# Performance work log

Measured on AMD Instinct MI355X. Metric: run time of the kernel, lower is better.

The kernel has to match this reference:

```python
import jax, jax.numpy as jnp
import numpy as np

N = 50000
E = 800000
IN_F, HID, OUT_F = 512, 256, 64
KEEP = 0.5  # Dropout(0.5)


def setup_inputs() -> dict:
    key = jax.random.key(0)
    ks = jax.random.split(key, 7)
    X = jax.random.normal(ks[0], (N, IN_F), dtype=jnp.float32)
    # Xavier-uniform-style init for the two layer weights
    lim1 = float(np.sqrt(6.0 / (IN_F + HID)))
    lim2 = float(np.sqrt(6.0 / (HID + OUT_F)))
    W1 = jax.random.uniform(ks[1], (IN_F, HID), jnp.float32, -lim1, lim1)
    W2 = jax.random.uniform(ks[2], (HID, OUT_F), jnp.float32, -lim2, lim2)
    a_row = jnp.sort(jax.random.randint(ks[3], (E,), 0, N)).astype(jnp.int64)
    a_col = jax.random.randint(ks[4], (E,), 0, N).astype(jnp.int64)
    a_val = jax.random.uniform(ks[5], (E,), jnp.float32)
    drop_mask = jax.random.randint(ks[6], (N, HID), 0, 2).astype(jnp.int32)
    return {"X": X, "W1": W1, "W2": W2, "a_row": a_row, "a_col": a_col,
            "a_val": a_val, "drop_mask": drop_mask}


def _spmm(a_row, a_col, a_val, dense):
    # A @ dense where A is [N, N] sparse in COO form: gather + weighted segment-sum
    msgs = a_val[:, None] * dense[a_col]          # [E, d]
    return jax.ops.segment_sum(msgs, a_row, num_segments=N)


def reference(X, W1, W2, a_row, a_col, a_val, drop_mask):
    # layer 1: feature transform + neighbor aggregation
    h = _spmm(a_row, a_col, a_val, X @ W1)        # [N, HID]
    h = jax.nn.relu(h)
    h = h * drop_mask.astype(h.dtype) * (1.0 / KEEP)  # Dropout(0.5), train mode
    # layer 2
    out = _spmm(a_row, a_col, a_val, h @ W2)      # [N, OUT_F]
    return jax.nn.log_softmax(out, axis=1)
```

## Files before the change

### kernel.cpp

```cpp
#include <hip/hip_runtime.h>
#include <hip/hip_bf16.h>
#include <math.h>

#define NN   50000
#define EE   800000
#define INF  512
#define HIDF 256
#define OUTF 64
#define MTILES (NN/16)

using short8 = __attribute__((ext_vector_type(8))) short;
using short4v = __attribute__((ext_vector_type(4))) short;
using f32x4  = __attribute__((ext_vector_type(4))) float;

typedef __attribute__((address_space(1))) const void gas_void;
typedef __attribute__((address_space(3))) void las_void;

static __device__ __forceinline__ short f2bf(float f){
  unsigned u = __builtin_bit_cast(unsigned, f);
  u += 0x7fff + ((u >> 16) & 1);
  return (short)(u >> 16);
}
static __device__ __forceinline__ float bf2f(short s){
  unsigned u = ((unsigned)(unsigned short)s) << 16;
  return __builtin_bit_cast(float, u);
}

__global__ void k_prep(const int* __restrict__ a_row, int* __restrict__ row_ptr,
                       const float* __restrict__ W1, short* __restrict__ W1p,
                       const float* __restrict__ W2, short* __restrict__ W2bT){
  int b = blockIdx.x, tid = threadIdx.x;
  if (b < 196){
    int i = b * 256 + tid;
    if (i > NN) return;
    int lo = 0, hi = EE;
    while (lo < hi){ int mid = (lo + hi) >> 1; if (a_row[mid] < i) lo = mid + 1; else hi = mid; }
    row_ptr[i] = lo;
  } else if (b < 708){
    int idx = (b - 196) * 256 + tid;
    int k = idx >> 8, col = idx & 255;
    int kk = k >> 5, k2 = k & 31;
    W1p[((kk << 8) + col) * 32 + k2] = f2bf(W1[idx]);
  } else {
    int idx = (b - 708) * 256 + tid;
    int k = idx >> 6, n = idx & 63;
    W2bT[n * HIDF + k] = f2bf(W2[idx]);
  }
}

__global__ __launch_bounds__(256) void k_gemm1(const float* __restrict__ X,
                                               const short* __restrict__ W1p,
                                               short* __restrict__ XW1b){
  __shared__ short lds[2][256 * 32];
  int wave = threadIdx.x >> 6, lane = threadIdx.x & 63;
  int l16 = lane & 15, quad = lane >> 4;
  int m0 = blockIdx.x * 64 + wave * 16;
  int r = min(m0 + l16, NN - 1);
  const float4* ap = (const float4*)(X + (size_t)r * INF + quad * 8);

  f32x4 acc[16];
  #pragma unroll
  for (int t = 0; t < 16; t++) acc[t] = (f32x4){0.f,0.f,0.f,0.f};

  auto stage = [&](int buf, int kk){
    const char* src = (const char*)(W1p + kk * (256 * 32));
    char* dst = (char*)&lds[buf][0];
    #pragma unroll
    for (int j = 0; j < 4; j++){
      int off = wave * 4096 + j * 1024;
      __builtin_amdgcn_global_load_lds((gas_void*)(src + off + lane * 16),
                                       (las_void*)(dst + off), 16, 0, 0);
    }
  };

  stage(0, 0);
  float4 a0 = ap[0], a1 = ap[1];
  __syncthreads();

  for (int kk = 0; kk < 16; kk++){
    int cur = kk & 1;
    float4 na0, na1;
    if (kk < 15){
      stage(cur ^ 1, kk + 1);
      na0 = ap[(kk + 1) * 8];
      na1 = ap[(kk + 1) * 8 + 1];
    }
    short8 af;
    af[0]=f2bf(a0.x); af[1]=f2bf(a0.y); af[2]=f2bf(a0.z); af[3]=f2bf(a0.w);
    af[4]=f2bf(a1.x); af[5]=f2bf(a1.y); af[6]=f2bf(a1.z); af[7]=f2bf(a1.w);
    const short* bp = &lds[cur][0] + l16 * 32 + quad * 8;
    #pragma unroll
    for (int nt = 0; nt < 16; nt++){
      short8 bf = *(const short8*)(bp + nt * 512);
      acc[nt] = __builtin_amdgcn_mfma_f32_16x16x32_bf16(af, bf, acc[nt], 0, 0, 0);
    }
    a0 = na0; a1 = na1;
    __syncthreads();
  }

  #pragma unroll
  for (int nt = 0; nt < 16; nt++){
    int col = nt*16 + l16;
    #pragma unroll
    for (int rr = 0; rr < 4; rr++){
      int row = m0 + quad*4 + rr;
      if (row < NN) XW1b[(size_t)row * HIDF + col] = f2bf(acc[nt][rr]);
    }
  }
}

__global__ __launch_bounds__(256) void k_spmm1(const int* __restrict__ row_ptr,
                                               const int* __restrict__ a_col,
                                               const float* __restrict__ a_val,
                                               const short* __restrict__ XW1b,
                                               const int* __restrict__ drop_mask,
                                               short* __restrict__ hb){
  int wave = threadIdx.x >> 6, lane = threadIdx.x & 63;
  int r = blockIdx.x * 4 + wave;
  int s = row_ptr[r], e = row_ptr[r+1];
  int g = lane >> 4;
  int c16 = lane & 15;
  float acc[16];
  #pragma unroll
  for (int j = 0; j < 16; j++) acc[j] = 0.f;

  int i = s + g;
  for (; i + 4 < e; i += 8){
    float v0 = a_val[i];     int c0 = a_col[i];
    float v1 = a_val[i+4];   int c1 = a_col[i+4];
    const short* p0 = XW1b + (size_t)c0 * HIDF + c16 * 16;
    const short* p1 = XW1b + (size_t)c1 * HIDF + c16 * 16;
    short8 x0a = *(const short8*)(p0);
    short8 x0b = *(const short8*)(p0 + 8);
    short8 x1a = *(const short8*)(p1);
    short8 x1b = *(const short8*)(p1 + 8);
    #pragma unroll
    for (int j = 0; j < 8; j++){
      acc[j]   += v0 * bf2f(x0a[j]);  acc[j+8] += v0 * bf2f(x0b[j]);
      acc[j]   += v1 * bf2f(x1a[j]);  acc[j+8] += v1 * bf2f(x1b[j]);
    }
  }
  for (; i < e; i += 4){
    float v = a_val[i];  int c = a_col[i];
    const short* p = XW1b + (size_t)c * HIDF + c16 * 16;
    short8 xa = *(const short8*)(p);
    short8 xb = *(const short8*)(p + 8);
    #pragma unroll
    for (int j = 0; j < 8; j++){
      acc[j] += v * bf2f(xa[j]);  acc[j+8] += v * bf2f(xb[j]);
    }
  }
  #pragma unroll
  for (int j = 0; j < 16; j++){
    acc[j] += __shfl_xor(acc[j], 16);
    acc[j] += __shfl_xor(acc[j], 32);
  }
  if (lane < 16){
    const int* dm = drop_mask + (size_t)r * HIDF + c16 * 16;
    short8 o0, o1;
    #pragma unroll
    for (int j = 0; j < 8; j++){
      o0[j] = f2bf(fmaxf(acc[j],   0.f) * (float)dm[j]   * 2.0f);
      o1[j] = f2bf(fmaxf(acc[j+8], 0.f) * (float)dm[j+8] * 2.0f);
    }
    short* hp = hb + (size_t)r * HIDF + c16 * 16;
    *(short8*)(hp)     = o0;
    *(short8*)(hp + 8) = o1;
  }
}

__global__ __launch_bounds__(256) void k_gemm2(const short* __restrict__ A,
                                               const short* __restrict__ BT,
                                               short* __restrict__ C){
  int wave = threadIdx.x >> 6, lane = threadIdx.x & 63;
  int tile_m = blockIdx.x * 4 + wave;
  if (tile_m >= MTILES) return;
  int m0 = tile_m * 16, l16 = lane & 15, quad = lane >> 4;

  f32x4 acc[4];
  #pragma unroll
  for (int t = 0; t < 4; t++) acc[t] = (f32x4){0.f,0.f,0.f,0.f};

  const short* ar = A + (size_t)(m0 + l16) * HIDF + quad * 8;
  for (int kk = 0; kk < HIDF/32; kk++){
    short8 af = *(const short8*)(ar + kk * 32);
    #pragma unroll
    for (int nt = 0; nt < 4; nt++){
      short8 bf = *(const short8*)(BT + (size_t)(nt*16 + l16) * HIDF + kk*32 + quad*8);
      acc[nt] = __builtin_amdgcn_mfma_f32_16x16x32_bf16(af, bf, acc[nt], 0, 0, 0);
    }
  }
  #pragma unroll
  for (int nt = 0; nt < 4; nt++){
    int col = nt*16 + l16;
    #pragma unroll
    for (int r = 0; r < 4; r++)
      C[(size_t)(m0 + quad*4 + r) * OUTF + col] = f2bf(acc[nt][r]);
  }
}

__global__ __launch_bounds__(256) void k_spmm2_lsm(const int* __restrict__ row_ptr,
                                                   const int* __restrict__ a_col,
                                                   const float* __restrict__ a_val,
                                                   const short* __restrict__ HW2b,
                                                   float* __restrict__ out){
  int wave = threadIdx.x >> 6, lane = threadIdx.x & 63;
  int r = blockIdx.x * 4 + wave;
  int s = row_ptr[r], e = row_ptr[r+1];
  int g = lane >> 4;
  int c4 = lane & 15;
  float acc[4] = {0,0,0,0};

  int i = s + g;
  for (; i + 4 < e; i += 8){
    float v0 = a_val[i];    int c0 = a_col[i];
    float v1 = a_val[i+4];  int c1 = a_col[i+4];
    short4v x0 = *(const short4v*)(HW2b + (size_t)c0 * OUTF + c4 * 4);
    short4v x1 = *(const short4v*)(HW2b + (size_t)c1 * OUTF + c4 * 4);
    #pragma unroll
    for (int j = 0; j < 4; j++){ acc[j] += v0 * bf2f(x0[j]); acc[j] += v1 * bf2f(x1[j]); }
  }
  for (; i < e; i += 4){
    float v = a_val[i];  int c = a_col[i];
    short4v x = *(const short4v*)(HW2b + (size_t)c * OUTF + c4 * 4);
    #pragma unroll
    for (int j = 0; j < 4; j++) acc[j] += v * bf2f(x[j]);
  }
  #pragma unroll
  for (int j = 0; j < 4; j++){
    acc[j] += __shfl_xor(acc[j], 16);
    acc[j] += __shfl_xor(acc[j], 32);
  }
  float m = fmaxf(fmaxf(acc[0], acc[1]), fmaxf(acc[2], acc[3]));
  #pragma unroll
  for (int o = 1; o <= 8; o <<= 1) m = fmaxf(m, __shfl_xor(m, o));
  float ssum = expf(acc[0]-m) + expf(acc[1]-m) + expf(acc[2]-m) + expf(acc[3]-m);
  #pragma unroll
  for (int o = 1; o <= 8; o <<= 1) ssum += __shfl_xor(ssum, o);
  float ls = logf(ssum);
  if (lane < 16){
    float4 o4 = { acc[0]-m-ls, acc[1]-m-ls, acc[2]-m-ls, acc[3]-m-ls };
    *(float4*)(out + (size_t)r * OUTF + c4 * 4) = o4;
  }
}

extern "C" void kernel_launch(void* const* d_in, const int* in_sizes, int n_in,
                              void* d_out, int out_size, void* d_ws, size_t ws_size,
                              hipStream_t stream) {
  const float* X      = (const float*)d_in[0];
  const float* W1     = (const float*)d_in[1];
  const float* W2     = (const float*)d_in[2];
  const int*   a_row  = (const int*)d_in[3];
  const int*   a_col  = (const int*)d_in[4];
  const float* a_val  = (const float*)d_in[5];
  const int*   drop   = (const int*)d_in[6];
  float*       out    = (float*)d_out;

  char* ws = (char*)d_ws;
  int*   row_ptr = (int*)  (ws);
  short* W1p     = (short*)(ws + 200704);
  short* W2bT    = (short*)(ws + 462848);
  short* XW1b    = (short*)(ws + 495616);
  short* hb      = (short*)(ws + 26095616);
  short* HW2b    = (short*)(ws + 51695616);

  k_prep<<<772, 256, 0, stream>>>(a_row, row_ptr, W1, W1p, W2, W2bT);
  k_gemm1<<<(NN + 63)/64, 256, 0, stream>>>(X, W1p, XW1b);
  k_spmm1<<<NN/4, 256, 0, stream>>>(row_ptr, a_col, a_val, XW1b, drop, hb);
  k_gemm2<<<(MTILES + 3)/4, 256, 0, stream>>>(hb, W2bT, HW2b);
  k_spmm2_lsm<<<NN/4, 256, 0, stream>>>(row_ptr, a_col, a_val, HW2b, out);
}
```

Baseline: 321.8 us.

## Software-pipeline SpMM gathers with three-deep register prefetch of neighbor rows

Rewrites both SpMM inner loops as a software pipeline that keeps two gathered rows in flight and prefetches the next column index and value a step ahead. Out-of-range slots clamp to a valid index and get a zero weight, so the separate remainder loop is no longer needed. The goal is to hide gather latency behind the FMAs. In exchange it uses more registers, issues redundant loads for masked slots, and may lower occupancy.

```diff
diff --git a/kernel.cpp b/kernel.cpp
--- a/kernel.cpp
+++ b/kernel.cpp
@@ -124,32 +124,44 @@
   #pragma unroll
   for (int j = 0; j < 16; j++) acc[j] = 0.f;
 
-  int i = s + g;
-  for (; i + 4 < e; i += 8){
-    float v0 = a_val[i];     int c0 = a_col[i];
-    float v1 = a_val[i+4];   int c1 = a_col[i+4];
+  int n = (e - s + 3) >> 2;
+
+  auto ldcv = [&](int t, float& v, int& c){
+    int idx = s + g + t * 4;
+    int ic = idx < e ? idx : (EE - 1);
+    float vv = a_val[ic];
+    c = a_col[ic];
+    v = idx < e ? vv : 0.f;
+  };
+
+  if (n > 0){
+    float v0, v1, v2; int c0, c1, c2;
+    ldcv(0, v0, c0);
     const short* p0 = XW1b + (size_t)c0 * HIDF + c16 * 16;
+    short8 xa0 = *(const short8*)(p0);
+    short8 xb0 = *(const short8*)(p0 + 8);
+    ldcv(1, v1, c1);
     const short* p1 = XW1b + (size_t)c1 * HIDF + c16 * 16;
-    short8 x0a = *(const short8*)(p0);
-    short8 x0b = *(const short8*)(p0 + 8);
-    short8 x1a = *(const short8*)(p1);
-    short8 x1b = *(const short8*)(p1 + 8);
-    #pragma unroll
-    for (int j = 0; j < 8; j++){
-      acc[j]   += v0 * bf2f(x0a[j]);  acc[j+8] += v0 * bf2f(x0b[j]);
-      acc[j]   += v1 * bf2f(x1a[j]);  acc[j+8] += v1 * bf2f(x1b[j]);
-    }
-  }
-  for (; i < e; i += 4){
-    float v = a_val[i];  int c = a_col[i];
-    const short* p = XW1b + (size_t)c * HIDF + c16 * 16;
-    short8 xa = *(const short8*)(p);
-    short8 xb = *(const short8*)(p + 8);
-    #pragma unroll
-    for (int j = 0; j < 8; j++){
-      acc[j] += v * bf2f(xa[j]);  acc[j+8] += v * bf2f(xb[j]);
-    }
-  }
+    short8 xa1 = *(const short8*)(p1);
+    short8 xb1 = *(const short8*)(p1 + 8);
+    ldcv(2, v2, c2);
+
+    for (int t = 0; t < n; t++){
+      const short* p2 = XW1b + (size_t)c2 * HIDF + c16 * 16;
+      short8 xa2 = *(const short8*)(p2);
+      short8 xb2 = *(const short8*)(p2 + 8);
+      float vn; int cn;
+      ldcv(t + 3, vn, cn);
+      #pragma unroll
+      for (int j = 0; j < 8; j++){
+        acc[j]   += v0 * bf2f(xa0[j]);
+        acc[j+8] += v0 * bf2f(xb0[j]);
+      }
+      xa0 = xa1; xb0 = xb1; xa1 = xa2; xb1 = xb2;
+      v0 = v1; v1 = v2; v2 = vn; c2 = cn;
+    }
+  }
+
   #pragma unroll
   for (int j = 0; j < 16; j++){
     acc[j] += __shfl_xor(acc[j], 16);
@@ -211,21 +223,35 @@
   int c4 = lane & 15;
   float acc[4] = {0,0,0,0};
 
-  int i = s + g;
-  for (; i + 4 < e; i += 8){
-    float v0 = a_val[i];    int c0 = a_col[i];
-    float v1 = a_val[i+4];  int c1 = a_col[i+4];
+  int n = (e - s + 3) >> 2;
+
+  auto ldcv = [&](int t, float& v, int& c){
+    int idx = s + g + t * 4;
+    int ic = idx < e ? idx : (EE - 1);
+    float vv = a_val[ic];
+    c = a_col[ic];
+    v = idx < e ? vv : 0.f;
+  };
+
+  if (n > 0){
+    float v0, v1, v2; int c0, c1, c2;
+    ldcv(0, v0, c0);
     short4v x0 = *(const short4v*)(HW2b + (size_t)c0 * OUTF + c4 * 4);
+    ldcv(1, v1, c1);
     short4v x1 = *(const short4v*)(HW2b + (size_t)c1 * OUTF + c4 * 4);
-    #pragma unroll
-    for (int j = 0; j < 4; j++){ acc[j] += v0 * bf2f(x0[j]); acc[j] += v1 * bf2f(x1[j]); }
-  }
-  for (; i < e; i += 4){
-    float v = a_val[i];  int c = a_col[i];
-    short4v x = *(const short4v*)(HW2b + (size_t)c * OUTF + c4 * 4);
-    #pragma unroll
-    for (int j = 0; j < 4; j++) acc[j] += v * bf2f(x[j]);
-  }
+    ldcv(2, v2, c2);
+
+    for (int t = 0; t < n; t++){
+      short4v x2 = *(const short4v*)(HW2b + (size_t)c2 * OUTF + c4 * 4);
+      float vn; int cn;
+      ldcv(t + 3, vn, cn);
+      #pragma unroll
+      for (int j = 0; j < 4; j++) acc[j] += v0 * bf2f(x0[j]);
+      x0 = x1; x1 = x2;
+      v0 = v1; v1 = v2; v2 = vn; c2 = cn;
+    }
+  }
+
   #pragma unroll
   for (int j = 0; j < 4; j++){
     acc[j] += __shfl_xor(acc[j], 16);
```

Result: no change. 321.3 us (-0.2%).
